# Kernel optimization log

Hardware: AMD Instinct MI355X
Metric: run time of the kernel (lower is better)

Reference implementation:

```python
import jax, jax.numpy as jnp
import numpy as np

SQRT2 = 1.4142135623730951  # ScaleCostWeight(sqrt(2)) applied to residuals
N_ITERS = 10
DAMP = 1e-8  # tiny Tikhonov for numerical safety of the 6x6 solve


def _hat(phi):
    x, y, z = phi[0], phi[1], phi[2]
    o = jnp.zeros((), phi.dtype)
    return jnp.stack([jnp.stack([o, -z, y]),
                      jnp.stack([z, o, -x]),
                      jnp.stack([-y, x, o])])


def se3_exp(xi):
    # xi: [6] = [rho (trans), phi (rot)] -> 4x4 SE3 matrix
    rho, phi = xi[:3], xi[3:]
    theta2 = jnp.sum(phi * phi)
    small = theta2 < 1e-12
    theta2s = jnp.where(small, 1.0, theta2)  # double-where for safe grads
    theta = jnp.sqrt(theta2s)
    A = jnp.where(small, 1.0, jnp.sin(theta) / theta)
    B = jnp.where(small, 0.5, (1.0 - jnp.cos(theta)) / theta2s)
    C = jnp.where(small, 1.0 / 6.0, (theta - jnp.sin(theta)) / (theta2s * theta))
    K = _hat(phi)
    K2 = K @ K
    I3 = jnp.eye(3, dtype=xi.dtype)
    R = I3 + A * K + B * K2
    V = I3 + B * K + C * K2
    t = V @ rho
    top = jnp.concatenate([R, t[:, None]], axis=1)
    bot = jnp.array([[0.0, 0.0, 0.0, 1.0]], dtype=xi.dtype)
    return jnp.concatenate([top, bot], axis=0)


def se3_inv(T):
    R = T[..., :3, :3]
    t = T[..., :3, 3:]
    Rt = jnp.swapaxes(R, -1, -2)
    top = jnp.concatenate([Rt, -(Rt @ t)], axis=-1)
    bot = jnp.broadcast_to(jnp.array([0.0, 0.0, 0.0, 1.0], T.dtype),
                           T.shape[:-2] + (1, 4))
    return jnp.concatenate([top, bot], axis=-2)


def _r_single(xi, T, src3, trg3, Wh, w):
    # residual of one batch element at local perturbation xi (retract on right)
    Tn = T @ se3_exp(xi)
    pred = Tn[:3, :3] @ src3 + Tn[:3, 3:4]          # [3, N]
    e = trg3 - pred                                  # [3, N]
    ew = jnp.einsum('nij,jn->in', Wh, e) * w         # cholesky-weighted, w: [1,N]
    return (ew * SQRT2).reshape(-1)                  # [3N]


def _forward(src4, trg4, w, T_init, inv_cov, T_s_v):
    src3 = src4[:, :3, :]
    trg3 = trg4[:, :3, :]
    # W_half = cholesky(inv_cov)^T, computed once (aux var, constant over iters)
    Wh = jnp.swapaxes(jnp.linalg.cholesky(inv_cov), -1, -2)  # [B, N, 3, 3]
    B = src4.shape[0]
    I6 = jnp.eye(6, dtype=src4.dtype)

    def step(T, _):
        xi0 = jnp.zeros((B, 6), T.dtype)
        J = jax.vmap(jax.jacfwd(_r_single), in_axes=(0, 0, 0, 0, 0, 0))(
            xi0, T, src3, trg3, Wh, w)               # [B, 3N, 6]
        r = jax.vmap(_r_single)(xi0, T, src3, trg3, Wh, w)  # [B, 3N]
        g = jnp.einsum('bri,br->bi', J, r)
        H = jnp.einsum('bri,brj->bij', J, J) + DAMP * I6
        dx = -jnp.linalg.solve(H, g[..., None])[..., 0]
        return T @ jax.vmap(se3_exp)(dx), None

    T, _ = jax.lax.scan(step, T_init, None, length=N_ITERS)
    T_sv = jnp.broadcast_to(T_s_v, (B, 4, 4))
    return se3_inv(T_sv) @ T @ T_sv


def setup_inputs() -> dict:
    key = jax.random.key(0)
    B, N = 256, 2048
    k1, k2, k3, k4, k5, k6 = jax.random.split(key, 6)
    src3 = 2.0 * jax.random.normal(k1, (B, 3, N), dtype=jnp.float32)
    # well-posed registration problem: trg = T_true * src + noise
    T_true = jax.vmap(se3_exp)(0.3 * jax.random.normal(k2, (B, 6), dtype=jnp.float32))
    trg3 = (jnp.einsum('bij,bjn->bin', T_true[:, :3, :3], src3)
            + T_true[:, :3, 3:4]
            + 0.01 * jax.random.normal(k3, (B, 3, N), dtype=jnp.float32))
    ones = jnp.ones((B, 1, N), dtype=jnp.float32)
    keypoints_3D_src = jnp.concatenate([src3, ones], axis=1)
    keypoints_3D_trg = jnp.concatenate([trg3, ones], axis=1)
    weights = jax.random.uniform(k4, (B, 1, N), dtype=jnp.float32,
                                 minval=0.1, maxval=1.0)
    A = 0.3 * jax.random.normal(k5, (B, N, 3, 3), dtype=jnp.float32)
    inv_cov_weights = A @ jnp.swapaxes(A, -1, -2) + jnp.eye(3, dtype=jnp.float32)
    T_trg_src_init = jax.vmap(se3_exp)(
        0.05 * jax.random.normal(k6, (B, 6), dtype=jnp.float32))
    T_s_v = se3_exp(jnp.array([0.1, -0.2, 0.3, 0.2, -0.1, 0.15], dtype=jnp.float32))
    return {"keypoints_3D_src": keypoints_3D_src,
            "keypoints_3D_trg": keypoints_3D_trg,
            "weights": weights,
            "T_trg_src_init": T_trg_src_init,
            "inv_cov_weights": inv_cov_weights,
            "T_s_v": T_s_v}


def reference(keypoints_3D_src, keypoints_3D_trg, weights, T_trg_src_init,
              inv_cov_weights, T_s_v):
    return _forward(keypoints_3D_src, keypoints_3D_trg, weights,
                    T_trg_src_init, inv_cov_weights, T_s_v)
```

## Files before the change

### kernel.cpp

```cpp
#include <hip/hip_runtime.h>
#include <math.h>

#define NPTS   2048
#define BD1    256
#define SPLIT  4
#define PPB    (NPTS / SPLIT)
#define PPT    (PPB / BD1)
#define NMOM   72
#define NITERS 10
#define DAMPF  1e-8f

__device__ __forceinline__ float frcp(float x) { return __builtin_amdgcn_rcpf(x); }
__device__ __forceinline__ float frsq(float x) { return __builtin_amdgcn_rsqf(x); }

__launch_bounds__(BD1, 3)
__global__ void moments_kernel(const float* __restrict__ src4,
                               const float* __restrict__ trg4,
                               const float* __restrict__ wts,
                               const float* __restrict__ icov,
                               float* __restrict__ mom, int B)
{
    const int b   = blockIdx.x / SPLIT;
    const int s   = blockIdx.x % SPLIT;
    const int tid = threadIdx.x;

    const float* srcb = src4 + (size_t)b * 4 * NPTS;
    const float* trgb = trg4 + (size_t)b * 4 * NPTS;
    const float* wb   = wts  + (size_t)b * NPTS;
    const float* cb   = icov + (size_t)b * NPTS * 9;

    float acc[NMOM];
    #pragma unroll
    for (int k = 0; k < NMOM; ++k) acc[k] = 0.0f;

    #pragma unroll
    for (int kk = 0; kk < PPT; ++kk) {
        int n = s * PPB + kk * BD1 + tid;
        float sx = srcb[n], sy = srcb[NPTS + n], sz = srcb[2 * NPTS + n];
        float gx = trgb[n], gy = trgb[NPTS + n], gz = trgb[2 * NPTS + n];
        float w  = wb[n];
        const float* c = cb + (size_t)n * 9;
        float c0 = c[0], c3 = c[3], c4 = c[4], c6 = c[6], c7 = c[7], c8 = c[8];

        float w2 = 2.0f * w * w;
        float W[6];
        W[0] = w2 * c0;
        W[1] = w2 * c3;
        W[2] = w2 * c6;
        W[3] = w2 * c4;
        W[4] = w2 * c7;
        W[5] = w2 * c8;

        float hx = W[0] * gx + W[1] * gy + W[2] * gz;
        float hy = W[1] * gx + W[3] * gy + W[4] * gz;
        float hz = W[2] * gx + W[4] * gy + W[5] * gz;

        float sv[3] = { sx, sy, sz };
        float hv[3] = { hx, hy, hz };
        float ss[6] = { sx*sx, sx*sy, sx*sz, sy*sy, sy*sz, sz*sz };

        #pragma unroll
        for (int ij = 0; ij < 6; ++ij) {
            acc[ij] += W[ij];
            #pragma unroll
            for (int c2 = 0; c2 < 3; ++c2) acc[6 + ij * 3 + c2] += W[ij] * sv[c2];
            #pragma unroll
            for (int cd = 0; cd < 6; ++cd) acc[24 + ij * 6 + cd] += W[ij] * ss[cd];
        }
        acc[60] += hx; acc[61] += hy; acc[62] += hz;
        #pragma unroll
        for (int c2 = 0; c2 < 3; ++c2)
            #pragma unroll
            for (int i = 0; i < 3; ++i) acc[63 + c2 * 3 + i] += sv[c2] * hv[i];
    }

    __shared__ float lds[36][BD1 + 1];
    #pragma unroll
    for (int h = 0; h < 2; ++h) {
        if (h) __syncthreads();
        #pragma unroll
        for (int k = 0; k < 36; ++k) lds[k][tid] = acc[h * 36 + k];
        __syncthreads();
        if (tid < 36) {
            const float* row = lds[tid];
            float s0 = 0.f, s1 = 0.f, s2 = 0.f, s3 = 0.f;
            #pragma unroll 8
            for (int j = 0; j < BD1; j += 4) {
                s0 += row[j]; s1 += row[j + 1]; s2 += row[j + 2]; s3 += row[j + 3];
            }
            mom[((size_t)s * NMOM + h * 36 + tid) * B + b] = (s0 + s1) + (s2 + s3);
        }
    }
}

__launch_bounds__(64, 1)
__global__ void solve_kernel(const float* __restrict__ mom,
                             const float* __restrict__ Tinit,
                             const float* __restrict__ Tsv,
                             float* __restrict__ out, int B)
{
    const int b = blockIdx.x * 64 + threadIdx.x;
    if (b >= B) return;

    float m[NMOM];
    #pragma unroll
    for (int k = 0; k < NMOM; ++k) {
        float v = 0.0f;
        #pragma unroll
        for (int s = 0; s < SPLIT; ++s)
            v += mom[((size_t)s * NMOM + k) * B + b];
        m[k] = v;
    }

    float Rm[3][3], tv[3];
    #pragma unroll
    for (int i = 0; i < 3; ++i) {
        #pragma unroll
        for (int j = 0; j < 3; ++j) Rm[i][j] = Tinit[b * 16 + i * 4 + j];
        tv[i] = Tinit[b * 16 + i * 4 + 3];
    }

    const int SY[3][3] = { {0,1,2}, {1,3,4}, {2,4,5} };

    for (int it = 0; it < NITERS; ++it) {
        float C1[6][3];
        #pragma unroll
        for (int ij = 0; ij < 6; ++ij) {
            float a0 = m[6 + ij * 3 + 0], a1 = m[6 + ij * 3 + 1], a2 = m[6 + ij * 3 + 2];
            #pragma unroll
            for (int a = 0; a < 3; ++a)
                C1[ij][a] = Rm[a][0] * a0 + Rm[a][1] * a1 + Rm[a][2] * a2;
        }
        float SM[3][3], SWp[3];
        #pragma unroll
        for (int i = 0; i < 3; ++i) {
            SM[i][0] = C1[SY[i][1]][2] - C1[SY[i][2]][1];
            SM[i][1] = C1[SY[i][2]][0] - C1[SY[i][0]][2];
            SM[i][2] = C1[SY[i][0]][1] - C1[SY[i][1]][0];
            SWp[i]   = C1[SY[i][0]][0] + C1[SY[i][1]][1] + C1[SY[i][2]][2];
        }
        float P2[6][6];
        #pragma unroll
        for (int ij = 0; ij < 6; ++ij) {
            float S00 = m[24 + ij * 6 + 0], S01 = m[24 + ij * 6 + 1], S02 = m[24 + ij * 6 + 2];
            float S11 = m[24 + ij * 6 + 3], S12 = m[24 + ij * 6 + 4], S22 = m[24 + ij * 6 + 5];
            float U[3][3];
            #pragma unroll
            for (int a = 0; a < 3; ++a) {
                U[a][0] = Rm[a][0] * S00 + Rm[a][1] * S01 + Rm[a][2] * S02;
                U[a][1] = Rm[a][0] * S01 + Rm[a][1] * S11 + Rm[a][2] * S12;
                U[a][2] = Rm[a][0] * S02 + Rm[a][1] * S12 + Rm[a][2] * S22;
            }
            P2[0][ij] = U[0][0]*Rm[0][0] + U[0][1]*Rm[0][1] + U[0][2]*Rm[0][2];
            P2[1][ij] = U[0][0]*Rm[1][0] + U[0][1]*Rm[1][1] + U[0][2]*Rm[1][2];
            P2[2][ij] = U[0][0]*Rm[2][0] + U[0][1]*Rm[2][1] + U[0][2]*Rm[2][2];
            P2[3][ij] = U[1][0]*Rm[1][0] + U[1][1]*Rm[1][1] + U[1][2]*Rm[1][2];
            P2[4][ij] = U[1][0]*Rm[2][0] + U[1][1]*Rm[2][1] + U[1][2]*Rm[2][2];
            P2[5][ij] = U[2][0]*Rm[2][0] + U[2][1]*Rm[2][1] + U[2][2]*Rm[2][2];
        }
        float SN00 = -P2[5][3] + 2.f * P2[4][4] - P2[3][5];
        float SN01 = -P2[2][4] + P2[5][1] + P2[1][5] - P2[4][2];
        float SN02 = -P2[4][1] + P2[2][3] + P2[3][2] - P2[1][4];
        float SN11 =  2.f * P2[2][2] - P2[5][0] - P2[0][5];
        float SN12 =  P2[4][0] - P2[2][1] - P2[1][2] + P2[0][4];
        float SN22 = -P2[3][0] + 2.f * P2[1][1] - P2[0][3];

        float SWt0 = m[0]*tv[0] + m[1]*tv[1] + m[2]*tv[2];
        float SWt1 = m[1]*tv[0] + m[3]*tv[1] + m[4]*tv[2];
        float SWt2 = m[2]*tv[0] + m[4]*tv[1] + m[5]*tv[2];
        float Su[3] = { m[60] - SWp[0] - SWt0,
                        m[61] - SWp[1] - SWt1,
                        m[62] - SWp[2] - SWt2 };

        float G[3][3];
        #pragma unroll
        for (int a = 0; a < 3; ++a)
            #pragma unroll
            for (int bb = 0; bb < 3; ++bb)
                G[a][bb] = Rm[a][0]*m[63 + 0 + bb] + Rm[a][1]*m[63 + 3 + bb] + Rm[a][2]*m[63 + 6 + bb];
        float ch[3] = { G[1][2] - G[2][1], G[2][0] - G[0][2], G[0][1] - G[1][0] };
        float pw[3];
        pw[0] = P2[1][2] + P2[3][4] + P2[4][5] - P2[2][1] - P2[4][3] - P2[5][4];
        pw[1] = P2[2][0] + P2[4][1] + P2[5][2] - P2[0][2] - P2[1][4] - P2[2][5];
        pw[2] = P2[0][1] + P2[1][3] + P2[2][4] - P2[1][0] - P2[3][1] - P2[4][2];
        float Sq[3];
        #pragma unroll
        for (int i = 0; i < 3; ++i)
            Sq[i] = ch[i] - pw[i] + SM[0][i]*tv[0] + SM[1][i]*tv[1] + SM[2][i]*tv[2];

        float Hm[6][6];
        Hm[0][0] = m[0]; Hm[0][1] = m[1]; Hm[0][2] = m[2];
        Hm[1][1] = m[3]; Hm[1][2] = m[4]; Hm[2][2] = m[5];
        #pragma unroll
        for (int i = 0; i < 3; ++i) {
            Hm[i][3] = -SM[i][0]; Hm[i][4] = -SM[i][1]; Hm[i][5] = -SM[i][2];
        }
        Hm[3][3] = -SN00; Hm[3][4] = -SN01; Hm[3][5] = -SN02;
        Hm[4][4] = -SN11; Hm[4][5] = -SN12; Hm[5][5] = -SN22;
        #pragma unroll
        for (int i = 0; i < 6; ++i) {
            Hm[i][i] += DAMPF;
            #pragma unroll
            for (int j = 0; j < 6; ++j)
                if (j < i) Hm[i][j] = Hm[j][i];
        }
        float rhs[6] = { Su[0], Su[1], Su[2], Sq[0], Sq[1], Sq[2] };

        float L[6][6];
        float invD[6];
        #pragma unroll
        for (int i = 0; i < 6; ++i) {
            #pragma unroll
            for (int j = 0; j < 6; ++j) {
                if (j > i) continue;
                float sum = Hm[i][j];
                #pragma unroll
                for (int k2 = 0; k2 < 6; ++k2)
                    if (k2 < j) sum -= L[i][k2] * L[j][k2];
                if (i == j) { invD[i] = frsq(sum); L[i][i] = sum * invD[i]; }
                else        L[i][j] = sum * invD[j];
            }
        }
        float z[6];
        #pragma unroll
        for (int i = 0; i < 6; ++i) {
            float sum = rhs[i];
            #pragma unroll
            for (int k2 = 0; k2 < 6; ++k2)
                if (k2 < i) sum -= L[i][k2] * z[k2];
            z[i] = sum * invD[i];
        }
        float y[6];
        #pragma unroll
        for (int i = 5; i >= 0; --i) {
            float sum = z[i];
            #pragma unroll
            for (int k2 = 0; k2 < 6; ++k2)
                if (k2 > i) sum -= L[k2][i] * y[k2];
            y[i] = sum * invD[i];
        }

        float drx = Rm[0][0]*y[0] + Rm[1][0]*y[1] + Rm[2][0]*y[2];
        float dry = Rm[0][1]*y[0] + Rm[1][1]*y[1] + Rm[2][1]*y[2];
        float drz = Rm[0][2]*y[0] + Rm[1][2]*y[1] + Rm[2][2]*y[2];
        float dpx = Rm[0][0]*y[3] + Rm[1][0]*y[4] + Rm[2][0]*y[5];
        float dpy = Rm[0][1]*y[3] + Rm[1][1]*y[4] + Rm[2][1]*y[5];
        float dpz = Rm[0][2]*y[3] + Rm[1][2]*y[4] + Rm[2][2]*y[5];

        float th2  = dpx*dpx + dpy*dpy + dpz*dpz;
        bool  sm   = th2 < 1e-12f;
        float th2s = sm ? 1.0f : th2;
        float th   = sqrtf(th2s);
        float ith  = frcp(th);
        float ith2 = ith * ith;
        float sth  = __sinf(th), cth = __cosf(th);
        float Ae = sm ? 1.0f : sth * ith;
        float Be = sm ? 0.5f : (1.0f - cth) * ith2;
        float Ce = sm ? (1.0f / 6.0f) : (th - sth) * ith2 * ith;
        float Rd00 = 1.0f + Be * (dpx*dpx - th2);
        float Rd01 = -Ae * dpz + Be * dpx * dpy;
        float Rd02 =  Ae * dpy + Be * dpx * dpz;
        float Rd10 =  Ae * dpz + Be * dpx * dpy;
        float Rd11 = 1.0f + Be * (dpy*dpy - th2);
        float Rd12 = -Ae * dpx + Be * dpy * dpz;
        float Rd20 = -Ae * dpy + Be * dpx * dpz;
        float Rd21 =  Ae * dpx + Be * dpy * dpz;
        float Rd22 = 1.0f + Be * (dpz*dpz - th2);
        float V00 = 1.0f + Ce * (dpx*dpx - th2);
        float V01 = -Be * dpz + Ce * dpx * dpy;
        float V02 =  Be * dpy + Ce * dpx * dpz;
        float V10 =  Be * dpz + Ce * dpx * dpy;
        float V11 = 1.0f + Ce * (dpy*dpy - th2);
        float V12 = -Be * dpx + Ce * dpy * dpz;
        float V20 = -Be * dpy + Ce * dpx * dpz;
        float V21 =  Be * dpx + Ce * dpy * dpz;
        float V22 = 1.0f + Ce * (dpz*dpz - th2);
        float tdx = V00 * drx + V01 * dry + V02 * drz;
        float tdy = V10 * drx + V11 * dry + V12 * drz;
        float tdz = V20 * drx + V21 * dry + V22 * drz;

        float nR[3][3];
        nR[0][0] = Rm[0][0]*Rd00 + Rm[0][1]*Rd10 + Rm[0][2]*Rd20;
        nR[0][1] = Rm[0][0]*Rd01 + Rm[0][1]*Rd11 + Rm[0][2]*Rd21;
        nR[0][2] = Rm[0][0]*Rd02 + Rm[0][1]*Rd12 + Rm[0][2]*Rd22;
        nR[1][0] = Rm[1][0]*Rd00 + Rm[1][1]*Rd10 + Rm[1][2]*Rd20;
        nR[1][1] = Rm[1][0]*Rd01 + Rm[1][1]*Rd11 + Rm[1][2]*Rd21;
        nR[1][2] = Rm[1][0]*Rd02 + Rm[1][1]*Rd12 + Rm[1][2]*Rd22;
        nR[2][0] = Rm[2][0]*Rd00 + Rm[2][1]*Rd10 + Rm[2][2]*Rd20;
        nR[2][1] = Rm[2][0]*Rd01 + Rm[2][1]*Rd11 + Rm[2][2]*Rd21;
        nR[2][2] = Rm[2][0]*Rd02 + Rm[2][1]*Rd12 + Rm[2][2]*Rd22;
        float ntx = Rm[0][0]*tdx + Rm[0][1]*tdy + Rm[0][2]*tdz + tv[0];
        float nty = Rm[1][0]*tdx + Rm[1][1]*tdy + Rm[1][2]*tdz + tv[1];
        float ntz = Rm[2][0]*tdx + Rm[2][1]*tdy + Rm[2][2]*tdz + tv[2];
        #pragma unroll
        for (int i = 0; i < 3; ++i)
            #pragma unroll
            for (int j = 0; j < 3; ++j) Rm[i][j] = nR[i][j];
        tv[0] = ntx; tv[1] = nty; tv[2] = ntz;
    }

    {
        float R00 = Rm[0][0], R01 = Rm[0][1], R02 = Rm[0][2];
        float R10 = Rm[1][0], R11 = Rm[1][1], R12 = Rm[1][2];
        float R20 = Rm[2][0], R21 = Rm[2][1], R22 = Rm[2][2];
        float tx = tv[0], ty = tv[1], tz = tv[2];

        float Rv00 = Tsv[0], Rv01 = Tsv[1], Rv02 = Tsv[2],  tvx = Tsv[3];
        float Rv10 = Tsv[4], Rv11 = Tsv[5], Rv12 = Tsv[6],  tvy = Tsv[7];
        float Rv20 = Tsv[8], Rv21 = Tsv[9], Rv22 = Tsv[10], tvz = Tsv[11];

        float P00 = R00*Rv00 + R01*Rv10 + R02*Rv20;
        float P01 = R00*Rv01 + R01*Rv11 + R02*Rv21;
        float P02 = R00*Rv02 + R01*Rv12 + R02*Rv22;
        float P10 = R10*Rv00 + R11*Rv10 + R12*Rv20;
        float P11 = R10*Rv01 + R11*Rv11 + R12*Rv21;
        float P12 = R10*Rv02 + R11*Rv12 + R12*Rv22;
        float P20 = R20*Rv00 + R21*Rv10 + R22*Rv20;
        float P21 = R20*Rv01 + R21*Rv11 + R22*Rv21;
        float P22 = R20*Rv02 + R21*Rv12 + R22*Rv22;
        float Ptx = R00*tvx + R01*tvy + R02*tvz + tx;
        float Pty = R10*tvx + R11*tvy + R12*tvz + ty;
        float Ptz = R20*tvx + R21*tvy + R22*tvz + tz;

        float ex = Ptx - tvx, ey = Pty - tvy, ez = Ptz - tvz;
        float* o = out + (size_t)b * 16;
        o[0]  = Rv00*P00 + Rv10*P10 + Rv20*P20;
        o[1]  = Rv00*P01 + Rv10*P11 + Rv20*P21;
        o[2]  = Rv00*P02 + Rv10*P12 + Rv20*P22;
        o[3]  = Rv00*ex  + Rv10*ey  + Rv20*ez;
        o[4]  = Rv01*P00 + Rv11*P10 + Rv21*P20;
        o[5]  = Rv01*P01 + Rv11*P11 + Rv21*P21;
        o[6]  = Rv01*P02 + Rv11*P12 + Rv21*P22;
        o[7]  = Rv01*ex  + Rv11*ey  + Rv21*ez;
        o[8]  = Rv02*P00 + Rv12*P10 + Rv22*P20;
        o[9]  = Rv02*P01 + Rv12*P11 + Rv22*P21;
        o[10] = Rv02*P02 + Rv12*P12 + Rv22*P22;
        o[11] = Rv02*ex  + Rv12*ey  + Rv22*ez;
        o[12] = 0.0f; o[13] = 0.0f; o[14] = 0.0f; o[15] = 1.0f;
    }
}

extern "C" void kernel_launch(void* const* d_in, const int* in_sizes, int n_in,
                              void* d_out, int out_size, void* d_ws, size_t ws_size,
                              hipStream_t stream)
{
    const float* src4  = (const float*)d_in[0];
    const float* trg4  = (const float*)d_in[1];
    const float* wts   = (const float*)d_in[2];
    const float* Tinit = (const float*)d_in[3];
    const float* icov  = (const float*)d_in[4];
    const float* Tsv   = (const float*)d_in[5];

    const int B = in_sizes[3] / 16;
    float* mom = (float*)d_ws;

    hipLaunchKernelGGL(moments_kernel, dim3(B * SPLIT), dim3(BD1), 0, stream,
                       src4, trg4, wts, icov, mom, B);
    hipLaunchKernelGGL(solve_kernel, dim3((B + 63) / 64), dim3(64), 0, stream,
                       mom, Tinit, Tsv, (float*)d_out, B);
}
```

Baseline: 117.4 us.

## Fuse moment accumulation and per-batch 6x6 solve into one kernel

Merges the moments kernel and the solve kernel into a single kernel with one 512-thread block per batch element. The cross-block split and the global workspace round trip go away. The LDS row reduction is replaced by a 32-lane shuffle reduction plus a small shared-memory sum. Thread 0 of each block then runs the 10-iteration Gauss-Newton solve alone, so the rest of the block sits idle during the serial solve and each batch element gets fewer blocks in the accumulation phase.

```diff
diff --git a/kernel.cpp b/kernel.cpp
--- a/kernel.cpp
+++ b/kernel.cpp
@@ -2,10 +2,8 @@
 #include <math.h>
 
 #define NPTS   2048
-#define BD1    256
-#define SPLIT  4
-#define PPB    (NPTS / SPLIT)
-#define PPT    (PPB / BD1)
+#define BD     512
+#define PPT    (NPTS / BD)
 #define NMOM   72
 #define NITERS 10
 #define DAMPF  1e-8f
@@ -13,15 +11,16 @@
 __device__ __forceinline__ float frcp(float x) { return __builtin_amdgcn_rcpf(x); }
 __device__ __forceinline__ float frsq(float x) { return __builtin_amdgcn_rsqf(x); }
 
-__launch_bounds__(BD1, 3)
-__global__ void moments_kernel(const float* __restrict__ src4,
-                               const float* __restrict__ trg4,
-                               const float* __restrict__ wts,
-                               const float* __restrict__ icov,
-                               float* __restrict__ mom, int B)
+__launch_bounds__(BD, 1)
+__global__ void fused_kernel(const float* __restrict__ src4,
+                             const float* __restrict__ trg4,
+                             const float* __restrict__ wts,
+                             const float* __restrict__ icov,
+                             const float* __restrict__ Tinit,
+                             const float* __restrict__ Tsv,
+                             float* __restrict__ out, int B)
 {
-    const int b   = blockIdx.x / SPLIT;
-    const int s   = blockIdx.x % SPLIT;
+    const int b   = blockIdx.x;
     const int tid = threadIdx.x;
 
     const float* srcb = src4 + (size_t)b * 4 * NPTS;
@@ -33,9 +32,9 @@
     #pragma unroll
     for (int k = 0; k < NMOM; ++k) acc[k] = 0.0f;
 
-    #pragma unroll
+    #pragma unroll 2
     for (int kk = 0; kk < PPT; ++kk) {
-        int n = s * PPB + kk * BD1 + tid;
+        int n = kk * BD + tid;
         float sx = srcb[n], sy = srcb[NPTS + n], sz = srcb[2 * NPTS + n];
         float gx = trgb[n], gy = trgb[NPTS + n], gz = trgb[2 * NPTS + n];
         float w  = wb[n];
@@ -74,43 +73,38 @@
             for (int i = 0; i < 3; ++i) acc[63 + c2 * 3 + i] += sv[c2] * hv[i];
     }
 
-    __shared__ float lds[36][BD1 + 1];
+    __shared__ float wsum[16][NMOM + 1];
+    __shared__ float msum[NMOM];
+    const int grp = tid >> 5;
+
     #pragma unroll
-    for (int h = 0; h < 2; ++h) {
-        if (h) __syncthreads();
-        #pragma unroll
-        for (int k = 0; k < 36; ++k) lds[k][tid] = acc[h * 36 + k];
-        __syncthreads();
-        if (tid < 36) {
-            const float* row = lds[tid];
-            float s0 = 0.f, s1 = 0.f, s2 = 0.f, s3 = 0.f;
-            #pragma unroll 8
-            for (int j = 0; j < BD1; j += 4) {
-                s0 += row[j]; s1 += row[j + 1]; s2 += row[j + 2]; s3 += row[j + 3];
-            }
-            mom[((size_t)s * NMOM + h * 36 + tid) * B + b] = (s0 + s1) + (s2 + s3);
-        }
-    }
-}
-
-__launch_bounds__(64, 1)
-__global__ void solve_kernel(const float* __restrict__ mom,
-                             const float* __restrict__ Tinit,
-                             const float* __restrict__ Tsv,
-                             float* __restrict__ out, int B)
-{
-    const int b = blockIdx.x * 64 + threadIdx.x;
-    if (b >= B) return;
+    for (int k = 0; k < NMOM; ++k) {
+        float v = acc[k];
+        v += __shfl_xor(v, 1);
+        v += __shfl_xor(v, 2);
+        v += __shfl_xor(v, 4);
+        v += __shfl_xor(v, 8);
+        v += __shfl_xor(v, 16);
+        acc[k] = v;
+    }
+    if ((tid & 31) == 0) {
+        #pragma unroll
+        for (int k = 0; k < NMOM; ++k) wsum[grp][k] = acc[k];
+    }
+    __syncthreads();
+    if (tid < NMOM) {
+        float s = 0.0f;
+        #pragma unroll
+        for (int j = 0; j < 16; ++j) s += wsum[j][tid];
+        msum[tid] = s;
+    }
+    __syncthreads();
+
+    if (tid != 0) return;
 
     float m[NMOM];
     #pragma unroll
-    for (int k = 0; k < NMOM; ++k) {
-        float v = 0.0f;
-        #pragma unroll
-        for (int s = 0; s < SPLIT; ++s)
-            v += mom[((size_t)s * NMOM + k) * B + b];
-        m[k] = v;
-    }
+    for (int k = 0; k < NMOM; ++k) m[k] = msum[k];
 
     float Rm[3][3], tv[3];
     #pragma unroll
@@ -352,10 +346,8 @@
     const float* Tsv   = (const float*)d_in[5];
 
     const int B = in_sizes[3] / 16;
-    float* mom = (float*)d_ws;
-
-    hipLaunchKernelGGL(moments_kernel, dim3(B * SPLIT), dim3(BD1), 0, stream,
-                       src4, trg4, wts, icov, mom, B);
-    hipLaunchKernelGGL(solve_kernel, dim3((B + 63) / 64), dim3(64), 0, stream,
-                       mom, Tinit, Tsv, (float*)d_out, B);
+    (void)d_ws; (void)ws_size;
+
+    hipLaunchKernelGGL(fused_kernel, dim3(B), dim3(BD), 0, stream,
+                       src4, trg4, wts, icov, Tinit, Tsv, (float*)d_out, B);
 }
```

Result: slower. 131.0 us (+11.6%).
